# Kernel optimization log

Measured on AMD Instinct MI355X. Metric: run time of the kernel, lower is better.

Reference implementation:

```python
import jax, jax.numpy as jnp
import numpy as np

KY, KX = 3, 3                      # kernel_size=(ky, kx)
PY, PX = (KY - 1) // 2, (KX - 1) // 2  # replicate padding per side (matches _compute_zero_padding2d)
CENTER = (KY * KX) // 2            # center tap, zeroed in the one-hot conv kernel


def setup_inputs() -> dict:
    key = jax.random.key(0)
    x = jax.random.normal(key, (8, 128, 256, 256), dtype=jnp.float32)
    return {"x": x}


def reference(x):
    # Faithful to kornia NonMaximaSuppression2d:
    #   1) replicate-pad by ((PY,PY),(PX,PX))
    #   2) gather the kx*ky neighborhood via one-hot conv (center tap weight = 0,
    #      so that channel is identically 0 and participates in the max)
    #   3) max over non-center neighbors (and the implicit 0), compare, mask-multiply
    B, C, H, W = x.shape
    xp = jnp.pad(x, ((0, 0), (0, 0), (PY, PY), (PX, PX)), mode="edge")
    # running max initialized to 0: replicates the all-zero center conv channel
    max_non_center = jnp.zeros_like(x)
    for i in range(KY):
        for j in range(KX):
            if i * KX + j == CENTER:
                continue
            max_non_center = jnp.maximum(max_non_center, xp[:, :, i:i + H, j:j + W])
    mask = x > max_non_center
    return x * mask.astype(x.dtype)
```

## Files before the change

kernel.cpp:

```cpp
#include <hip/hip_runtime.h>


#define NMS_W 256
#define NMS_H 256
#define ROWS 8

__global__ __launch_bounds__(256) void nms2d_kernel(
    const float* __restrict__ x, float* __restrict__ out) {
    const int lane = threadIdx.x & 63;
    const int wid  = threadIdx.x >> 6;
    const int gid  = blockIdx.x;
    const int blocksPerPlane = (NMS_H / ROWS) / 4;
    const long plane = gid / blocksPerPlane;
    const int  chunk = gid % blocksPerPlane;
    const int  row0  = (chunk * 4 + wid) * ROWS;

    const float* p = x   + plane * (long)(NMS_H * NMS_W);
    float*       q = out + plane * (long)(NMS_H * NMS_W);

    const int c0 = lane * 4;
    const int cl = (c0 == 0) ? 0 : c0 - 1;
    const int cr = (c0 == NMS_W - 4) ? NMS_W - 1 : c0 + 4;

    float t[6], m[6], b[6];
    auto load6 = [&](int r, float* a) {
        const float* rp = p + (long)r * NMS_W;
        const float4 v = *reinterpret_cast<const float4*>(rp + c0);
        a[0] = rp[cl]; a[1] = v.x; a[2] = v.y; a[3] = v.z; a[4] = v.w; a[5] = rp[cr];
    };

    load6(row0 == 0 ? 0 : row0 - 1, t);
    load6(row0, m);

#pragma unroll
    for (int r = 0; r < ROWS; ++r) {
        int rb = row0 + r + 1;
        if (rb > NMS_H - 1) rb = NMS_H - 1;
        load6(rb, b);

        float4 o;
        float* op = &o.x;
#pragma unroll
        for (int k = 0; k < 4; ++k) {
            float mx = fmaxf(fmaxf(t[k], t[k + 1]), t[k + 2]);
            mx = fmaxf(mx, fmaxf(m[k], m[k + 2]));
            mx = fmaxf(mx, fmaxf(fmaxf(b[k], b[k + 1]), b[k + 2]));
            mx = fmaxf(mx, 0.0f);
            const float c = m[k + 1];
            op[k] = (c > mx) ? c : 0.0f;
        }
        *reinterpret_cast<float4*>(q + (long)(row0 + r) * NMS_W + c0) = o;

#pragma unroll
        for (int k = 0; k < 6; ++k) { t[k] = m[k]; m[k] = b[k]; }
    }
}

extern "C" void kernel_launch(void* const* d_in, const int* in_sizes, int n_in,
                              void* d_out, int out_size, void* d_ws, size_t ws_size,
                              hipStream_t stream) {
    const float* x = (const float*)d_in[0];
    float* out = (float*)d_out;
    const int planes = out_size / (NMS_H * NMS_W);
    const int grid = planes * ((NMS_H / ROWS) / 4);
    nms2d_kernel<<<grid, 256, 0, stream>>>(x, out);
}
```

Before: 99.94 us.

## Use wavefront shuffles for horizontal halo and double rows per wave

Replaces the two scalar halo loads per row with cross-lane shuffles of precomputed column maxima, so each row costs one float4 load. It also factors the 3x3 max into column maxima to cut ALU work, and doubles rows per wave to 16, which reduces the vertical halo reload overhead. The trade-off is half as many blocks and thus less parallelism, which may reduce latency hiding on a memory-bound kernel.

```diff
diff --git a/kernel.cpp b/kernel.cpp
--- a/kernel.cpp
+++ b/kernel.cpp
@@ -3,7 +3,7 @@
 
 #define NMS_W 256
 #define NMS_H 256
-#define ROWS 8
+#define ROWS 16
 
 __global__ __launch_bounds__(256) void nms2d_kernel(
     const float* __restrict__ x, float* __restrict__ out) {
@@ -17,42 +17,46 @@
 
     const float* p = x   + plane * (long)(NMS_H * NMS_W);
     float*       q = out + plane * (long)(NMS_H * NMS_W);
+    const int c0 = lane * 4;
 
-    const int c0 = lane * 4;
-    const int cl = (c0 == 0) ? 0 : c0 - 1;
-    const int cr = (c0 == NMS_W - 4) ? NMS_W - 1 : c0 + 4;
-
-    float t[6], m[6], b[6];
-    auto load6 = [&](int r, float* a) {
-        const float* rp = p + (long)r * NMS_W;
-        const float4 v = *reinterpret_cast<const float4*>(rp + c0);
-        a[0] = rp[cl]; a[1] = v.x; a[2] = v.y; a[3] = v.z; a[4] = v.w; a[5] = rp[cr];
-    };
-
-    load6(row0 == 0 ? 0 : row0 - 1, t);
-    load6(row0, m);
+    float4 t = *reinterpret_cast<const float4*>(
+        p + (long)(row0 == 0 ? 0 : row0 - 1) * NMS_W + c0);
+    float4 m = *reinterpret_cast<const float4*>(p + (long)row0 * NMS_W + c0);
 
 #pragma unroll
     for (int r = 0; r < ROWS; ++r) {
         int rb = row0 + r + 1;
         if (rb > NMS_H - 1) rb = NMS_H - 1;
-        load6(rb, b);
+        const float4 b = *reinterpret_cast<const float4*>(
+            p + (long)rb * NMS_W + c0);
+
+        const float cm0 = fmaxf(fmaxf(t.x, m.x), b.x);
+        const float cm1 = fmaxf(fmaxf(t.y, m.y), b.y);
+        const float cm2 = fmaxf(fmaxf(t.z, m.z), b.z);
+        const float cm3 = fmaxf(fmaxf(t.w, m.w), b.w);
+        const float tb0 = fmaxf(t.x, b.x);
+        const float tb1 = fmaxf(t.y, b.y);
+        const float tb2 = fmaxf(t.z, b.z);
+        const float tb3 = fmaxf(t.w, b.w);
+
+        float left  = __shfl_up(cm3, 1);
+        float right = __shfl_down(cm0, 1);
+        if (lane == 0)  left  = cm0;
+        if (lane == 63) right = cm3;
+
+        const float n0 = fmaxf(fmaxf(fmaxf(left, tb0), cm1), 0.0f);
+        const float n1 = fmaxf(fmaxf(fmaxf(cm0,  tb1), cm2), 0.0f);
+        const float n2 = fmaxf(fmaxf(fmaxf(cm1,  tb2), cm3), 0.0f);
+        const float n3 = fmaxf(fmaxf(fmaxf(cm2,  tb3), right), 0.0f);
 
         float4 o;
-        float* op = &o.x;
-#pragma unroll
-        for (int k = 0; k < 4; ++k) {
-            float mx = fmaxf(fmaxf(t[k], t[k + 1]), t[k + 2]);
-            mx = fmaxf(mx, fmaxf(m[k], m[k + 2]));
-            mx = fmaxf(mx, fmaxf(fmaxf(b[k], b[k + 1]), b[k + 2]));
-            mx = fmaxf(mx, 0.0f);
-            const float c = m[k + 1];
-            op[k] = (c > mx) ? c : 0.0f;
-        }
+        o.x = (m.x > n0) ? m.x : 0.0f;
+        o.y = (m.y > n1) ? m.y : 0.0f;
+        o.z = (m.z > n2) ? m.z : 0.0f;
+        o.w = (m.w > n3) ? m.w : 0.0f;
         *reinterpret_cast<float4*>(q + (long)(row0 + r) * NMS_W + c0) = o;
 
-#pragma unroll
-        for (int k = 0; k < 6; ++k) { t[k] = m[k]; m[k] = b[k]; }
+        t = m; m = b;
     }
 }
 
```

After: 103.7 us. 1.04x slower.
